# Performance work log

Measured on AMD Instinct MI355X. Metric: run time of the kernel, lower is better.

## Reference

```python
import jax, jax.numpy as jnp
import numpy as np

HIDDEN = 768
HEADS = 12
HEAD_DIM = HIDDEN // HEADS
SCALE = HEAD_DIM ** -0.5
GAMMA = 0.5  # non-trainable nn.Parameter in the original module


def setup_inputs() -> dict:
    key = jax.random.key(0)
    k1, k2, k3, k4 = jax.random.split(key, 4)
    B, N, C = 2, 2048, HIDDEN
    x = jax.random.normal(k1, (B, N, C), dtype=jnp.float32)
    w_qkv = jax.random.normal(k2, (3 * C, C), dtype=jnp.float32) * 0.02
    w_out = jax.random.normal(k3, (C, C), dtype=jnp.float32) * 0.02
    b_out = jax.random.normal(k4, (C,), dtype=jnp.float32) * 0.02
    return {"x": x, "w_qkv": w_qkv, "w_out": w_out, "b_out": b_out}


def _spa_mask(N: int, dtype) -> jnp.ndarray:
    # has_cls=False path: mask[k, j] = GAMMA iff j % (N//4) == k % (N//4), else 1.
    NUM = N // 4
    rows = jnp.arange(N) % NUM  # [N]
    cols = jnp.arange(N) % NUM  # [N]
    return jnp.where(rows[:, None] == cols[None, :],
                     jnp.asarray(GAMMA, dtype), jnp.asarray(1.0, dtype))  # [N, N]


def reference(x, w_qkv, w_out, b_out):
    B, N, C = x.shape
    H, D = HEADS, HEAD_DIM
    # qkv projection (no bias): [B,N,3C] -> [3,B,H,N,D] per 'b n (qkv h d) -> qkv b h n d'
    qkv = jnp.einsum('bnc,fc->bnf', x, w_qkv).reshape(B, N, 3, H, D)
    qkv = jnp.transpose(qkv, (2, 0, 3, 1, 4))
    q, k, v = qkv[0], qkv[1], qkv[2]
    # first softmax over scaled scores
    att = jax.nn.softmax(jnp.einsum('bhxd,bhyd->bhxy', q, k) * SCALE, axis=-1)
    # structured block-periodic mask multiply, then second softmax
    mask = _spa_mask(N, att.dtype)  # [N,N], broadcasts over [B,H,N,N]
    att = jax.nn.softmax(att * mask, axis=-1)
    # value weighting and output projection
    out = jnp.einsum('bhxy,bhyd->bhxd', att, v)  # [B,H,N,D]
    out = jnp.transpose(out, (0, 2, 1, 3)).reshape(B, N, C)  # b h n d -> b n (h d)
    return jnp.einsum('bnc,oc->bno', out, w_out) + b_out
```

## Files before the change

kernel.cpp:

```cpp
#include <hip/hip_runtime.h>
#include <hip/hip_bf16.h>
#include <cstdint>
#include <cstddef>

typedef __attribute__((ext_vector_type(8))) short short8;
typedef __attribute__((ext_vector_type(4))) short short4v;
typedef __attribute__((ext_vector_type(4))) float f32x4;
typedef __attribute__((ext_vector_type(16))) float f32x16;

#define HH 12
#define DD 64
#define NN 2048
#define CC 768
#define QSCALE 0.18033688011112042f

#if defined(__has_builtin)
#if __has_builtin(__builtin_amdgcn_global_load_lds)
#define HAVE_GLOAD_LDS 1
#endif
#endif

#ifdef HAVE_GLOAD_LDS
#define GL16(gp, lp)                                                         \
  __builtin_amdgcn_global_load_lds(                                         \
      (__attribute__((address_space(1))) void*)(size_t)(const void*)(gp),   \
      (__attribute__((address_space(3))) void*)(lp), 16, 0, 0)
#endif

__device__ __forceinline__ float bf2f(short s) {
  union { uint32_t u; float f; } v;
  v.u = ((uint32_t)(uint16_t)s) << 16;
  return v.f;
}
__device__ __forceinline__ short f2bf(float f) {
  union { float f; uint32_t u; } v; v.f = f;
  uint32_t r = v.u + 0x7FFFu + ((v.u >> 16) & 1u);
  return (short)(r >> 16);
}
__device__ __forceinline__ uint32_t cvtpk(float a, float b) {
  uint32_t r;
  asm("v_cvt_pk_bf16_f32 %0, %1, %2" : "=v"(r) : "v"(a), "v"(b));
  return r;
}
__device__ __forceinline__ float exp2raw(float x) {
  float r;
  asm("v_exp_f32 %0, %1" : "=v"(r) : "v"(x));
  return r;
}

__global__ __launch_bounds__(256)
void norm_k(const float* __restrict__ s0, const float* __restrict__ s1,
            const float* __restrict__ s2,
            short* __restrict__ d0, short* __restrict__ d1,
            short* __restrict__ d2)
{
  const int bid = blockIdx.x;
  const float* src; short* dst; int base;
  if (bid < 1536)      { src = s0; dst = d0; base = bid; }
  else if (bid < 2400) { src = s1; dst = d1; base = bid - 1536; }
  else                 { src = s2; dst = d2; base = bid - 2400; }
  const int idx = (base * 256 + (int)threadIdx.x) * 8;
  const float* sf = src + idx;
  f32x4 a = *(const f32x4*)sf;
  f32x4 b = *(const f32x4*)(sf + 4);
  short8 o;
  o[0] = f2bf(a[0]); o[1] = f2bf(a[1]); o[2] = f2bf(a[2]); o[3] = f2bf(a[3]);
  o[4] = f2bf(b[0]); o[5] = f2bf(b[1]); o[6] = f2bf(b[2]); o[7] = f2bf(b[3]);
  *(short8*)(dst + idx) = o;
}

template <int MODE>
__global__ __launch_bounds__(256, 2)
void gemm_k(const short* __restrict__ A, const short* __restrict__ W,
            const float* __restrict__ bias,
            short* __restrict__ O0, short* __restrict__ O1, short* __restrict__ O2,
            float* __restrict__ Of)
{
  __shared__ __align__(16) short lA[128 * 64];
  __shared__ __align__(16) short lB[128 * 64];
  const int tid = threadIdx.x;
  const int w = tid >> 6, l = tid & 63;
  const int lq = l & 15, lh = l >> 4;
  const int m0 = blockIdx.y * 128;
  const int f0 = blockIdx.x * 128;

#ifdef HAVE_GLOAD_LDS
  const int lrow = l >> 3;
  const int gseg = ((l & 7) ^ lrow) * 8;
#else
  const int seg = tid & 7;
  const int rbase = tid >> 3;
#endif

  f32x4 acc[4][4] = {};

  for (int kb = 0; kb < CC; kb += 64) {
    __syncthreads();
#ifdef HAVE_GLOAD_LDS
#pragma unroll
    for (int j = 0; j < 4; ++j) {
      const int rw = j * 32 + w * 8;
      const int row = rw + lrow;
      GL16(A + (size_t)(m0 + row) * CC + kb + gseg, &lA[rw * 64]);
      GL16(W + (size_t)(f0 + row) * CC + kb + gseg, &lB[rw * 64]);
    }
#else
#pragma unroll
    for (int j = 0; j < 4; ++j) {
      const int row = j * 32 + rbase;
      const int dst = row * 128 + ((seg * 16) ^ ((row & 7) << 4));
      *(short8*)((char*)lA + dst) =
          *(const short8*)(A + (size_t)(m0 + row) * CC + kb + seg * 8);
      *(short8*)((char*)lB + dst) =
          *(const short8*)(W + (size_t)(f0 + row) * CC + kb + seg * 8);
    }
#endif
    __syncthreads();
    const int wr = (w >> 1) * 64, wc = (w & 1) * 64;
#pragma unroll
    for (int c = 0; c < 2; ++c) {
      short8 af[4], bfr[4];
#pragma unroll
      for (int i = 0; i < 4; ++i) {
        const int rowA = wr + i * 16 + lq;
        af[i] = *(const short8*)((char*)lA + rowA * 128 +
                                 ((c * 64 + lh * 16) ^ ((rowA & 7) << 4)));
        const int rowB = wc + i * 16 + lq;
        bfr[i] = *(const short8*)((char*)lB + rowB * 128 +
                                  ((c * 64 + lh * 16) ^ ((rowB & 7) << 4)));
      }
#pragma unroll
      for (int mi = 0; mi < 4; ++mi)
#pragma unroll
        for (int ni = 0; ni < 4; ++ni)
          acc[mi][ni] = __builtin_amdgcn_mfma_f32_16x16x32_bf16(
              af[mi], bfr[ni], acc[mi][ni], 0, 0, 0);
    }
  }

  const int wr = (w >> 1) * 64, wc = (w & 1) * 64;
#pragma unroll
  for (int ni = 0; ni < 4; ++ni) {
    const int fb = f0 + wc + ni * 16;
    if (MODE == 0) {
      const int which = fb / CC;
      const int hd = fb - which * CC;
      const int h = hd >> 6;
      const int d = (hd & 63) + lq;
#pragma unroll
      for (int mi = 0; mi < 4; ++mi) {
        const int mb = m0 + wr + mi * 16 + 4 * lh;
        const int b = mb >> 11;
        const int n = mb & 2047;
        if (which == 0) {
#pragma unroll
          for (int r = 0; r < 4; ++r)
            O0[(((size_t)(b * HH + h) * NN) + n + r) * DD + d] =
                f2bf(acc[mi][ni][r] * QSCALE);
        } else if (which == 1) {
#pragma unroll
          for (int r = 0; r < 4; ++r)
            O1[(((size_t)(b * HH + h) * NN) + n + r) * DD + d] =
                f2bf(acc[mi][ni][r]);
        } else {
          short4v pk;
#pragma unroll
          for (int r = 0; r < 4; ++r) pk[r] = f2bf(acc[mi][ni][r]);
          *(short4v*)(O2 + ((size_t)(b * HH + h) * DD + d) * NN + n) = pk;
        }
      }
    } else {
      const float bv = bias[fb + lq];
#pragma unroll
      for (int mi = 0; mi < 4; ++mi) {
        const int mb = m0 + wr + mi * 16 + 4 * lh;
#pragma unroll
        for (int r = 0; r < 4; ++r)
          Of[(size_t)(mb + r) * CC + fb + lq] = acc[mi][ni][r] + bv;
      }
    }
  }
}

__global__ __launch_bounds__(256)
void colsum_k(const short* __restrict__ VT, float* __restrict__ cs)
{
  const int bh = blockIdx.x, t = threadIdx.x;
  const int d = t >> 2, part = t & 3;
  const short* p = VT + ((size_t)bh * DD + d) * NN + part * 512;
  float s = 0.f;
  for (int i = 0; i < 512; i += 8) {
    short8 v = *(const short8*)(p + i);
#pragma unroll
    for (int e = 0; e < 8; ++e) s += bf2f(v[e]);
  }
  s += __shfl_xor(s, 1);
  s += __shfl_xor(s, 2);
  if (part == 0) cs[bh * DD + d] = s;
}

#define EXPPACK(sacc_, pa_, l1a_, l1b_, mc_, qwoff_)                         \
  do {                                                                       \
    uint32_t dw[8];                                                          \
    if ((((qw + (qwoff_)) - kb) & 511) == 0) {                               \
      const int mreg = (((lq >> 2) & 1) == hi)                               \
                           ? ((lq & 3) | (((lq >> 3) & 3) << 2)) : -1;       \
      _Pragma("unroll")                                                      \
      for (int j2 = 0; j2 < 8; ++j2) {                                       \
        float e0 = exp2raw(sacc_[2 * j2]);                                   \
        float e1 = exp2raw(sacc_[2 * j2 + 1]);                               \
        l1a_ += e0; l1b_ += e1;                                              \
        mc_ += (2 * j2 == mreg) ? e0 : 0.f;                                  \
        mc_ += (2 * j2 + 1 == mreg) ? e1 : 0.f;                              \
        e0 = (2 * j2 == mreg) ? 0.5f * e0 : e0;                              \
        e1 = (2 * j2 + 1 == mreg) ? 0.5f * e1 : e1;                          \
        dw[j2] = cvtpk(e0, e1);                                              \
      }                                                                      \
    } else {                                                                 \
      _Pragma("unroll")                                                      \
      for (int j2 = 0; j2 < 8; ++j2) {                                       \
        const float e0 = exp2raw(sacc_[2 * j2]);                             \
        const float e1 = exp2raw(sacc_[2 * j2 + 1]);                         \
        l1a_ += e0; l1b_ += e1;                                              \
        dw[j2] = cvtpk(e0, e1);                                              \
      }                                                                      \
    }                                                                        \
    _Pragma("unroll")                                                        \
    for (int half = 0; half < 2; ++half) {                                   \
      uint32_t a0 = dw[4 * half + 0], a1 = dw[4 * half + 1];                 \
      uint32_t a2 = dw[4 * half + 2], a3 = dw[4 * half + 3];                 \
      asm("v_permlane32_swap_b32 %0, %1" : "+v"(a0), "+v"(a2));              \
      asm("v_permlane32_swap_b32 %0, %1" : "+v"(a1), "+v"(a3));              \
      union { uint32_t u4[4]; short8 s; } pk;                                \
      pk.u4[0] = a0; pk.u4[1] = a1; pk.u4[2] = a2; pk.u4[3] = a3;            \
      pa_[half] = pk.s;                                                      \
    }                                                                        \
  } while (0)

__global__ __launch_bounds__(256, 3)
void attn_k(const short* __restrict__ Qb, const short* __restrict__ Kb,
            const short* __restrict__ VT, const float* __restrict__ cs,
            short* __restrict__ AO)
{
  __shared__ __align__(16) char smem[50688];
  float* comb  = (float*)smem;
  float* combL = (float*)(smem + 49152);
  float* combM = (float*)(smem + 49152 + 768);

  const int tid = threadIdx.x;
  const int kc = tid >> 6, l = tid & 63;
  const int lq = l & 31, hi = l >> 5;

  const int bid = (int)blockIdx.x;
  const int sbid = (bid & 7) * 96 + (bid >> 3);
  const int bh = sbid >> 5;
  const int qsub = sbid & 31;

  const short* Qh = Qb + (size_t)bh * NN * DD;
  const short* Kh = Kb + (size_t)bh * NN * DD;
  const short* Vh = VT + (size_t)bh * DD * NN;

  const int qw = qsub * 64;

  short8 qf0[4], qf1[4];
#pragma unroll
  for (int c = 0; c < 4; ++c) {
    qf0[c] = *(const short8*)(Qh + (size_t)(qw + lq) * DD + c * 16 + hi * 8);
    qf1[c] = *(const short8*)(Qh + (size_t)(qw + 32 + lq) * DD + c * 16 + hi * 8);
  }

  f32x16 pv0[2] = {}, pv1[2] = {};
  float l1a0 = 0.f, l1b0 = 0.f, mc0 = 0.f;
  float l1a1 = 0.f, l1b1 = 0.f, mc1 = 0.f;

  const int cbase = kc * 8192;
  const int kb0 = kc * (NN / 4);
  const short* Kc = Kh + (size_t)kb0 * DD;
  const short* Vc = Vh + kb0;

#ifdef HAVE_GLOAD_LDS
  int gK[4], gV[4];
#pragma unroll
  for (int j = 0; j < 4; ++j) {
    const int rowK = j * 8 + (l >> 3);
    gK[j] = rowK * DD + (((l & 7) ^ (l >> 3)) * 8);
    const int rowV = j * 16 + (l >> 2);
    gV[j] = rowV * NN + (((l & 3) ^ ((l >> 3) & 3)) * 8);
  }
#define SK(t_)                                                               \
  do {                                                                       \
    _Pragma("unroll")                                                        \
    for (int j = 0; j < 4; ++j)                                              \
      GL16(Kc + (size_t)(t_) * 32 * DD + gK[j], smem + cbase + j * 1024);    \
  } while (0)
#define SV(t_)                                                               \
  do {                                                                       \
    _Pragma("unroll")                                                        \
    for (int j = 0; j < 4; ++j)                                              \
      GL16(Vc + (t_) * 32 + gV[j], smem + cbase + 4096 + j * 1024);          \
  } while (0)
#else
  int sdK[4], sgK[4], sdV[4], sgV[4];
#pragma unroll
  for (int j = 0; j < 4; ++j) {
    const int rowK = j * 8 + (l >> 3);
    sdK[j] = cbase + rowK * 128 + (((l & 7) * 16) ^ ((rowK & 7) << 4));
    sgK[j] = rowK * DD + (l & 7) * 8;
    const int rowV = j * 16 + (l >> 2);
    sdV[j] = cbase + 4096 + rowV * 64 + (((l & 3) * 16) ^ (((rowV >> 1) & 3) << 4));
    sgV[j] = rowV * NN + (l & 3) * 8;
  }
#define SK(t_)                                                               \
  do {                                                                       \
    _Pragma("unroll")                                                        \
    for (int j = 0; j < 4; ++j)                                              \
      *(short8*)(smem + sdK[j]) =                                            \
          *(const short8*)(Kc + (size_t)(t_) * 32 * DD + sgK[j]);            \
  } while (0)
#define SV(t_)                                                               \
  do {                                                                       \
    _Pragma("unroll")                                                        \
    for (int j = 0; j < 4; ++j)                                              \
      *(short8*)(smem + sdV[j]) =                                            \
          *(const short8*)(Vc + (t_) * 32 + sgV[j]);                         \
  } while (0)
#endif

  int kaddr[4], vaddr[4];
#pragma unroll
  for (int c = 0; c < 4; ++c)
    kaddr[c] = cbase + lq * 128 + (((c * 2 + hi) * 16) ^ ((lq & 7) << 4));
#pragma unroll
  for (int ch = 0; ch < 2; ++ch)
#pragma unroll
    for (int dg = 0; dg < 2; ++dg) {
      const int rowV = dg * 32 + lq;
      vaddr[ch * 2 + dg] = cbase + 4096 + rowV * 64 +
                           (((ch * 2 + hi) * 16) ^ (((rowV >> 1) & 3) << 4));
    }

  SK(0);
  SV(0);

  for (int t = 0; t < 16; ++t) {
    const int kb = kb0 + t * 32;
#ifdef HAVE_GLOAD_LDS
    asm volatile("s_waitcnt vmcnt(4)" ::: "memory");
    __builtin_amdgcn_sched_barrier(0);
#else
    asm volatile("s_waitcnt lgkmcnt(0)" ::: "memory");
#endif

    f32x16 sacc0 = {}, sacc1 = {};
    __builtin_amdgcn_s_setprio(1);
#pragma unroll
    for (int c = 0; c < 4; ++c) {
      short8 kf = *(const short8*)(smem + kaddr[c]);
      sacc0 = __builtin_amdgcn_mfma_f32_32x32x16_bf16(kf, qf0[c], sacc0, 0, 0, 0);
      sacc1 = __builtin_amdgcn_mfma_f32_32x32x16_bf16(kf, qf1[c], sacc1, 0, 0, 0);
    }
    __builtin_amdgcn_s_setprio(0);
    asm volatile("s_waitcnt lgkmcnt(0)" ::: "memory");
    if (t + 1 < 16) SK(t + 1);

    short8 pa0[2], pa1[2];
    EXPPACK(sacc0, pa0, l1a0, l1b0, mc0, 0);
    EXPPACK(sacc1, pa1, l1a1, l1b1, mc1, 32);

#ifdef HAVE_GLOAD_LDS
    asm volatile("s_waitcnt vmcnt(4)" ::: "memory");
    __builtin_amdgcn_sched_barrier(0);
#endif

    __builtin_amdgcn_s_setprio(1);
#pragma unroll
    for (int ch = 0; ch < 2; ++ch)
#pragma unroll
      for (int dg = 0; dg < 2; ++dg) {
        short8 vf = *(const short8*)(smem + vaddr[ch * 2 + dg]);
        pv0[dg] = __builtin_amdgcn_mfma_f32_32x32x16_bf16(pa0[ch], vf, pv0[dg], 0, 0, 0);
        pv1[dg] = __builtin_amdgcn_mfma_f32_32x32x16_bf16(pa1[ch], vf, pv1[dg], 0, 0, 0);
      }
    __builtin_amdgcn_s_setprio(0);
    asm volatile("s_waitcnt lgkmcnt(0)" ::: "memory");
    if (t + 1 < 16) SV(t + 1);
  }

  float l1s[2], mcs[2];
  l1s[0] = l1a0 + l1b0;  l1s[0] += __shfl_xor(l1s[0], 32);
  l1s[1] = l1a1 + l1b1;  l1s[1] += __shfl_xor(l1s[1], 32);
  mcs[0] = mc0 + __shfl_xor(mc0, 32);
  mcs[1] = mc1 + __shfl_xor(mc1, 32);

  __syncthreads();
  if (kc) {
    float* pb = comb + (kc - 1) * 4096;
#pragma unroll
    for (int dg = 0; dg < 2; ++dg)
#pragma unroll
      for (int r = 0; r < 16; ++r) {
        const int qrow = (r & 3) + 8 * (r >> 2) + 4 * hi;
        pb[qrow * 64 + dg * 32 + lq] = pv0[dg][r];
        pb[(32 + qrow) * 64 + dg * 32 + lq] = pv1[dg][r];
      }
    if (hi == 0) {
      combL[(kc - 1) * 64 + lq]      = l1s[0];
      combL[(kc - 1) * 64 + 32 + lq] = l1s[1];
      combM[(kc - 1) * 64 + lq]      = mcs[0];
      combM[(kc - 1) * 64 + 32 + lq] = mcs[1];
    }
  }
  __syncthreads();
  if (kc == 0) {
    const int b = bh / HH, h = bh - b * HH;
#pragma unroll
    for (int s = 0; s < 2; ++s) {
      const float l1t = l1s[s] + combL[s * 32 + lq] + combL[64 + s * 32 + lq] +
                        combL[128 + s * 32 + lq];
      const float mct = mcs[s] + combM[s * 32 + lq] + combM[64 + s * 32 + lq] +
                        combM[128 + s * 32 + lq];
      const float s1t = l1t - 0.5f * mct;
#pragma unroll
      for (int r = 0; r < 16; ++r) {
        const int qrow = (r & 3) + 8 * (r >> 2) + 4 * hi;
        const float l1r = __shfl(l1t, qrow);
        const float s1r = __shfl(s1t, qrow);
        const float rden = 1.f / (2048.f * l1r + s1r);
        const int n = qw + s * 32 + qrow;
#pragma unroll
        for (int dg = 0; dg < 2; ++dg) {
          const int d = dg * 32 + lq;
          const float pvt = (s ? pv1[dg][r] : pv0[dg][r]) +
                            comb[(s * 32 + qrow) * 64 + d] +
                            comb[4096 + (s * 32 + qrow) * 64 + d] +
                            comb[8192 + (s * 32 + qrow) * 64 + d];
          const float csv = cs[bh * DD + d];
          AO[((size_t)(b * NN + n)) * CC + h * DD + d] =
              f2bf((csv * l1r + pvt) * rden);
        }
      }
    }
  }
}

extern "C" void kernel_launch(void* const* d_in, const int* in_sizes, int n_in,
                              void* d_out, int out_size, void* d_ws, size_t ws_size,
                              hipStream_t stream)
{
  (void)in_sizes; (void)n_in; (void)out_size;
  float* out = (float*)d_out;

  const size_t HD = (size_t)2 * HH * NN * DD;
  const size_t NX = 3145728, NW = 1769472, NO = 589824;
  const size_t need = (4 * HD + NX + NW + NO) * sizeof(short)
                    + (size_t)2 * HH * DD * sizeof(float) + 64;
  if (ws_size < need) return;

  short* Qb = (short*)d_ws;
  short* Kb = Qb + HD;
  short* VT = Kb + HD;
  short* AO = VT + HD;
  float* cs = (float*)(AO + HD);
  short* xb  = (short*)(cs + 2 * HH * DD);
  short* wqb = xb + NX;
  short* wob = wqb + NW;

  dim3 blk(256);
  norm_k<<<dim3(2688), blk, 0, stream>>>((const float*)d_in[0],
                                         (const float*)d_in[1],
                                         (const float*)d_in[2],
                                         xb, wqb, wob);
  gemm_k<0><<<dim3(2304 / 128, 4096 / 128), blk, 0, stream>>>(
      xb, wqb, nullptr, Qb, Kb, VT, nullptr);
  colsum_k<<<dim3(2 * HH), blk, 0, stream>>>(VT, cs);
  attn_k<<<dim3(24 * 32), blk, 0, stream>>>(Qb, Kb, VT, cs, AO);
  gemm_k<1><<<dim3(CC / 128, 4096 / 128), blk, 0, stream>>>(
      AO, wob, (const float*)d_in[3], nullptr, nullptr, nullptr, out);
}
```

Before: 105.5 us.

## Double-buffer K tiles in attention and add smaller-tile output projection GEMM

The attention kernel now keeps two K tile buffers in LDS, prefetching tile t+2 while tile t is consumed. Wait counts are relaxed so global-to-LDS loads stay further ahead of the MFMA work. Separately, the output projection gets a dedicated 64x64-tile GEMM kernel, giving more blocks for better CU occupancy on the small N=768 problem. The cost is more LDS per attention block (wrap-around prefetches of unused tiles at the end) and possibly lower reuse per block in the output GEMM.

```diff
diff --git a/kernel.cpp b/kernel.cpp
--- a/kernel.cpp
+++ b/kernel.cpp
@@ -178,6 +178,87 @@
         for (int r = 0; r < 4; ++r)
           Of[(size_t)(mb + r) * CC + fb + lq] = acc[mi][ni][r] + bv;
       }
+    }
+  }
+}
+
+__global__ __launch_bounds__(256, 4)
+void gemm1_k(const short* __restrict__ A, const short* __restrict__ W,
+             const float* __restrict__ bias, float* __restrict__ Of)
+{
+  __shared__ __align__(16) short lA[64 * 64];
+  __shared__ __align__(16) short lB[64 * 64];
+  const int tid = threadIdx.x;
+  const int w = tid >> 6, l = tid & 63;
+  const int lq = l & 15, lh = l >> 4;
+  const int m0 = blockIdx.y * 64;
+  const int f0 = blockIdx.x * 64;
+
+#ifdef HAVE_GLOAD_LDS
+  const int lrow = l >> 3;
+  const int gseg = ((l & 7) ^ lrow) * 8;
+#else
+  const int seg = tid & 7;
+  const int rbase = tid >> 3;
+#endif
+
+  f32x4 acc[2][2] = {};
+
+  for (int kb = 0; kb < CC; kb += 64) {
+    __syncthreads();
+#ifdef HAVE_GLOAD_LDS
+#pragma unroll
+    for (int j = 0; j < 2; ++j) {
+      const int rw = j * 32 + w * 8;
+      const int row = rw + lrow;
+      GL16(A + (size_t)(m0 + row) * CC + kb + gseg, &lA[rw * 64]);
+      GL16(W + (size_t)(f0 + row) * CC + kb + gseg, &lB[rw * 64]);
+    }
+#else
+#pragma unroll
+    for (int j = 0; j < 2; ++j) {
+      const int row = j * 32 + rbase;
+      const int dst = row * 128 + ((seg * 16) ^ ((row & 7) << 4));
+      *(short8*)((char*)lA + dst) =
+          *(const short8*)(A + (size_t)(m0 + row) * CC + kb + seg * 8);
+      *(short8*)((char*)lB + dst) =
+          *(const short8*)(W + (size_t)(f0 + row) * CC + kb + seg * 8);
+    }
+#endif
+    __syncthreads();
+    const int wr = (w >> 1) * 32, wc = (w & 1) * 32;
+#pragma unroll
+    for (int c = 0; c < 2; ++c) {
+      short8 af[2], bfr[2];
+#pragma unroll
+      for (int i = 0; i < 2; ++i) {
+        const int rowA = wr + i * 16 + lq;
+        af[i] = *(const short8*)((char*)lA + rowA * 128 +
+                                 ((c * 64 + lh * 16) ^ ((rowA & 7) << 4)));
+        const int rowB = wc + i * 16 + lq;
+        bfr[i] = *(const short8*)((char*)lB + rowB * 128 +
+                                  ((c * 64 + lh * 16) ^ ((rowB & 7) << 4)));
+      }
+#pragma unroll
+      for (int mi = 0; mi < 2; ++mi)
+#pragma unroll
+        for (int ni = 0; ni < 2; ++ni)
+          acc[mi][ni] = __builtin_amdgcn_mfma_f32_16x16x32_bf16(
+              af[mi], bfr[ni], acc[mi][ni], 0, 0, 0);
+    }
+  }
+
+  const int wr = (w >> 1) * 32, wc = (w & 1) * 32;
+#pragma unroll
+  for (int ni = 0; ni < 2; ++ni) {
+    const int fb = f0 + wc + ni * 16;
+    const float bv = bias[fb + lq];
+#pragma unroll
+    for (int mi = 0; mi < 2; ++mi) {
+      const int mb = m0 + wr + mi * 16 + 4 * lh;
+#pragma unroll
+      for (int r = 0; r < 4; ++r)
+        Of[(size_t)(mb + r) * CC + fb + lq] = acc[mi][ni][r] + bv;
     }
   }
 }
@@ -273,7 +354,7 @@
   float l1a0 = 0.f, l1b0 = 0.f, mc0 = 0.f;
   float l1a1 = 0.f, l1b1 = 0.f, mc1 = 0.f;
 
-  const int cbase = kc * 8192;
+  const int cbase = kc * 12288;
   const int kb0 = kc * (NN / 4);
   const short* Kc = Kh + (size_t)kb0 * DD;
   const short* Vc = Vh + kb0;
@@ -287,17 +368,18 @@
     const int rowV = j * 16 + (l >> 2);
     gV[j] = rowV * NN + (((l & 3) ^ ((l >> 3) & 3)) * 8);
   }
-#define SK(t_)                                                               \
+#define SK(t_, boff_)                                                        \
   do {                                                                       \
     _Pragma("unroll")                                                        \
     for (int j = 0; j < 4; ++j)                                              \
-      GL16(Kc + (size_t)(t_) * 32 * DD + gK[j], smem + cbase + j * 1024);    \
+      GL16(Kc + (size_t)(t_) * 32 * DD + gK[j],                              \
+           smem + cbase + (boff_) + j * 1024);                               \
   } while (0)
 #define SV(t_)                                                               \
   do {                                                                       \
     _Pragma("unroll")                                                        \
     for (int j = 0; j < 4; ++j)                                              \
-      GL16(Vc + (t_) * 32 + gV[j], smem + cbase + 4096 + j * 1024);          \
+      GL16(Vc + (t_) * 32 + gV[j], smem + cbase + 8192 + j * 1024);          \
   } while (0)
 #else
   int sdK[4], sgK[4], sdV[4], sgV[4];
@@ -307,14 +389,14 @@
     sdK[j] = cbase + rowK * 128 + (((l & 7) * 16) ^ ((rowK & 7) << 4));
     sgK[j] = rowK * DD + (l & 7) * 8;
     const int rowV = j * 16 + (l >> 2);
-    sdV[j] = cbase + 4096 + rowV * 64 + (((l & 3) * 16) ^ (((rowV >> 1) & 3) << 4));
+    sdV[j] = cbase + 8192 + rowV * 64 + (((l & 3) * 16) ^ (((rowV >> 1) & 3) << 4));
     sgV[j] = rowV * NN + (l & 3) * 8;
   }
-#define SK(t_)                                                               \
+#define SK(t_, boff_)                                                        \
   do {                                                                       \
     _Pragma("unroll")                                                        \
     for (int j = 0; j < 4; ++j)                                              \
-      *(short8*)(smem + sdK[j]) =                                            \
+      *(short8*)(smem + (boff_) + sdK[j]) =                                  \
           *(const short8*)(Kc + (size_t)(t_) * 32 * DD + sgK[j]);            \
   } while (0)
 #define SV(t_)                                                               \
@@ -335,19 +417,27 @@
 #pragma unroll
     for (int dg = 0; dg < 2; ++dg) {
       const int rowV = dg * 32 + lq;
-      vaddr[ch * 2 + dg] = cbase + 4096 + rowV * 64 +
+      vaddr[ch * 2 + dg] = cbase + 8192 + rowV * 64 +
                            (((ch * 2 + hi) * 16) ^ (((rowV >> 1) & 3) << 4));
     }
 
-  SK(0);
+#ifdef HAVE_GLOAD_LDS
+  SK(0, 0);
   SV(0);
+  SK(1, 4096);
+#else
+  SK(0, 0);
+  SV(0);
+#endif
 
   for (int t = 0; t < 16; ++t) {
     const int kb = kb0 + t * 32;
 #ifdef HAVE_GLOAD_LDS
-    asm volatile("s_waitcnt vmcnt(4)" ::: "memory");
+    const int koff = (t & 1) * 4096;
+    asm volatile("s_waitcnt vmcnt(8)" ::: "memory");
     __builtin_amdgcn_sched_barrier(0);
 #else
+    const int koff = 0;
     asm volatile("s_waitcnt lgkmcnt(0)" ::: "memory");
 #endif
 
@@ -355,13 +445,16 @@
     __builtin_amdgcn_s_setprio(1);
 #pragma unroll
     for (int c = 0; c < 4; ++c) {
-      short8 kf = *(const short8*)(smem + kaddr[c]);
+      short8 kf = *(const short8*)(smem + koff + kaddr[c]);
       sacc0 = __builtin_amdgcn_mfma_f32_32x32x16_bf16(kf, qf0[c], sacc0, 0, 0, 0);
       sacc1 = __builtin_amdgcn_mfma_f32_32x32x16_bf16(kf, qf1[c], sacc1, 0, 0, 0);
     }
     __builtin_amdgcn_s_setprio(0);
     asm volatile("s_waitcnt lgkmcnt(0)" ::: "memory");
-    if (t + 1 < 16) SK(t + 1);
+    __builtin_amdgcn_sched_barrier(0);
+#ifdef HAVE_GLOAD_LDS
+    SK((t + 2) & 15, koff);
+#endif
 
     short8 pa0[2], pa1[2];
     EXPPACK(sacc0, pa0, l1a0, l1b0, mc0, 0);
@@ -383,7 +476,12 @@
       }
     __builtin_amdgcn_s_setprio(0);
     asm volatile("s_waitcnt lgkmcnt(0)" ::: "memory");
-    if (t + 1 < 16) SV(t + 1);
+    __builtin_amdgcn_sched_barrier(0);
+#ifdef HAVE_GLOAD_LDS
+    SV((t + 1) & 15);
+#else
+    if (t + 1 < 16) { SK(t + 1, 0); SV(t + 1); }
+#endif
   }
 
   float l1s[2], mcs[2];
@@ -474,6 +572,6 @@
       xb, wqb, nullptr, Qb, Kb, VT, nullptr);
   colsum_k<<<dim3(2 * HH), blk, 0, stream>>>(VT, cs);
   attn_k<<<dim3(24 * 32), blk, 0, stream>>>(Qb, Kb, VT, cs, AO);
-  gemm_k<1><<<dim3(CC / 128, 4096 / 128), blk, 0, stream>>>(
-      AO, wob, (const float*)d_in[3], nullptr, nullptr, nullptr, out);
-}
+  gemm1_k<<<dim3(CC / 64, 4096 / 64), blk, 0, stream>>>(
+      AO, wob, (const float*)d_in[3], out);
+}
```

After: 99.96 us (median of 2 runs). 1.06x faster.
